# Kernel optimization log

Hardware: AMD Instinct MI355X
Metric: run time of the kernel (lower is better)

The kernel has to match this reference:

```python
import jax, jax.numpy as jnp
import numpy as np

B, T, LIE, OBS = 8, 2048, 32, 64
D = 2 * LIE  # d_head


def setup_inputs() -> dict:
    key = jax.random.key(0)
    ks = jax.random.split(key, 12)
    positions = jax.random.normal(ks[0], (B, T, D, D), dtype=jnp.float32)
    content_emb = jax.random.normal(ks[1], (B, T, OBS), dtype=jnp.float32)
    F = jnp.eye(LIE, dtype=jnp.float32) + 0.01 * jax.random.normal(ks[2], (LIE, LIE), dtype=jnp.float32)
    log_Q_diag = 0.1 * jax.random.normal(ks[3], (LIE,), dtype=jnp.float32)
    log_R_diag = 0.1 * jax.random.normal(ks[4], (OBS,), dtype=jnp.float32)
    H_w = jax.random.normal(ks[5], (OBS, LIE), dtype=jnp.float32) * (1.0 / np.sqrt(LIE))
    det_w1 = jax.random.normal(ks[6], (64, OBS), dtype=jnp.float32) * (1.0 / np.sqrt(OBS))
    det_b1 = jnp.zeros((64,), dtype=jnp.float32)
    det_w2 = jax.random.normal(ks[7], (1, 64), dtype=jnp.float32) * (1.0 / 8.0)
    det_b2 = jnp.zeros((1,), dtype=jnp.float32)
    obs_w = jax.random.normal(ks[8], (OBS, OBS), dtype=jnp.float32) * (1.0 / np.sqrt(OBS))
    obs_b = jnp.zeros((OBS,), dtype=jnp.float32)
    return {"positions": positions, "content_emb": content_emb, "F": F,
            "log_Q_diag": log_Q_diag, "log_R_diag": log_R_diag, "H_w": H_w,
            "det_w1": det_w1, "det_b1": det_b1, "det_w2": det_w2, "det_b2": det_b2,
            "obs_w": obs_w, "obs_b": obs_b}


def reference(positions, content_emb, F, log_Q_diag, log_R_diag, H_w,
              det_w1, det_b1, det_w2, det_b2, obs_w, obs_b):
    Bn, Tn, d, _ = positions.shape
    L = log_Q_diag.shape[0]
    Qd = jnp.exp(log_Q_diag)            # (L,) process noise diag
    Rd = jnp.exp(log_R_diag)            # (O,) measurement noise diag
    # landmark detector MLP + sigmoid (all timesteps at once)
    h = jax.nn.relu(content_emb @ det_w1.T + det_b1)
    probs = jax.nn.sigmoid((h @ det_w2.T + det_b2)[..., 0])   # (B,T)
    z_all = content_emb @ obs_w.T + obs_b                      # (B,T,O)
    ar = jnp.arange(L)
    I_L = jnp.eye(L, dtype=positions.dtype)
    Sigma0 = jnp.broadcast_to(I_L * 0.01, (Bn, L, L))

    def step(Sigma, inp):
        pos_t, z_t, prob_t = inp  # (B,d,d), (B,O), (B,)
        # predict: F Sigma F^T + Q
        Sigma = jnp.einsum('ij,bjk,lk->bil', F, Sigma, F) + jnp.diag(Qd)[None]
        # extract diagonal 2x2 blocks -> (B,L,2,2)
        resh = pos_t.reshape(Bn, L, 2, L, 2).transpose(0, 1, 3, 2, 4)  # (B,L,L,2,2)
        blocks = resh[:, ar, ar]
        # log map SO(2): theta = atan2(R10, R00)
        mu = jnp.arctan2(blocks[..., 1, 0], blocks[..., 0, 0])  # (B,L)
        # Kalman update
        S = jnp.einsum('oi,bij,pj->bop', H_w, Sigma, H_w) + jnp.diag(Rd)[None]
        K = jnp.einsum('bij,oj,bop->bip', Sigma, H_w, jnp.linalg.inv(S))  # (B,L,O)
        y = z_t - mu @ H_w.T
        mu_c = mu + jnp.einsum('bio,bo->bi', K, y)
        IKH = I_L[None] - K @ H_w
        Sigma_u = jnp.einsum('bij,bjk,blk->bil', IKH, Sigma, IKH) \
                  + jnp.einsum('bio,o,bjo->bij', K, Rd, K)
        # exp map SO(2)
        c, s = jnp.cos(mu_c), jnp.sin(mu_c)
        nb = jnp.stack([jnp.stack([c, -s], -1), jnp.stack([s, c], -1)], -2)  # (B,L,2,2)
        gate = jnp.any(prob_t > 0.5)  # torch branch: update only if any landmark
        a4 = prob_t[:, None, None, None]
        blended = jnp.where(gate, a4 * nb + (1.0 - a4) * blocks, blocks)
        a3 = prob_t[:, None, None]
        Sigma_out = jnp.where(gate, a3 * Sigma_u + (1.0 - a3) * Sigma, Sigma)
        corr_t = resh.at[:, ar, ar].set(blended).transpose(0, 1, 3, 2, 4).reshape(Bn, d, d)
        return Sigma_out, (corr_t, Sigma_out)

    _, (corr, covs) = jax.lax.scan(
        step, Sigma0,
        (positions.transpose(1, 0, 2, 3), z_all.transpose(1, 0, 2), probs.T))
    return corr.transpose(1, 0, 2, 3), covs.transpose(1, 0, 2, 3), probs
```

## Files before the change

kernel.cpp:

```cpp
#include <hip/hip_runtime.h>
#include <math.h>

#define TT 2048
#define NB 8
#define CH 16
#define BURN 32
#define NCH (TT / CH)
#define WMAX (BURN + CH)

typedef __attribute__((ext_vector_type(16))) float f32x16;
typedef __attribute__((ext_vector_type(8))) __bf16 bf16x8;

__device__ __forceinline__ bf16x8 ph(const f32x16& x, int base) {
  bf16x8 r;
#pragma unroll
  for (int d = 0; d < 8; ++d) r[d] = (__bf16)x[base + d];
  return r;
}
__device__ __forceinline__ bf16x8 pl(const f32x16& x, int base) {
  bf16x8 r;
#pragma unroll
  for (int d = 0; d < 8; ++d) {
    float t = x[base + d];
    r[d] = (__bf16)(t - (float)((__bf16)t));
  }
  return r;
}
struct FragsH { bf16x8 h0, h1; };
struct Frags { bf16x8 h0, l0, h1, l1; };
__device__ __forceinline__ FragsH mkh(const f32x16& x) { return {ph(x, 0), ph(x, 8)}; }
__device__ __forceinline__ Frags mkf(const f32x16& x) {
  return {ph(x, 0), pl(x, 0), ph(x, 8), pl(x, 8)};
}

#define MFMA_B __builtin_amdgcn_mfma_f32_32x32x16_bf16
__device__ __forceinline__ f32x16 mmA(bf16x8 a0, bf16x8 a1, bf16x8 b0, bf16x8 b1, f32x16 c) {
  c = MFMA_B(a0, b0, c, 0, 0, 0);
  c = MFMA_B(a1, b1, c, 0, 0, 0);
  return c;
}
__device__ __forceinline__ f32x16 mm6(const Frags& A, const Frags& B, f32x16 c) {
  f32x16 u = {};
  c = MFMA_B(A.h0, B.h0, c, 0, 0, 0);  u = MFMA_B(A.h0, B.l0, u, 0, 0, 0);
  c = MFMA_B(A.h1, B.h1, c, 0, 0, 0);  u = MFMA_B(A.h1, B.l1, u, 0, 0, 0);
  c = MFMA_B(A.l0, B.h0, c, 0, 0, 0);  u = MFMA_B(A.l1, B.h1, u, 0, 0, 0);
  return c + u;
}

__global__ __launch_bounds__(256) void k_setup(const float* __restrict__ Hw,
                                               const float* __restrict__ logR,
                                               float* __restrict__ cinv,
                                               float* __restrict__ htr) {
  __shared__ float C[32][33];
  __shared__ float rinv[64];
  int tid = threadIdx.x;
  if (tid < 64) rinv[tid] = expf(-logR[tid]);
  __syncthreads();
  int i = tid >> 3, j0 = (tid & 7) << 2;
  float a0 = 0.f, a1 = 0.f, a2 = 0.f, a3 = 0.f;
  for (int o = 0; o < 64; ++o) {
    float hio = Hw[o * 32 + i] * rinv[o];
    a0 += hio * Hw[o * 32 + j0];
    a1 += hio * Hw[o * 32 + j0 + 1];
    a2 += hio * Hw[o * 32 + j0 + 2];
    a3 += hio * Hw[o * 32 + j0 + 3];
  }
  C[i][j0] = a0; C[i][j0 + 1] = a1; C[i][j0 + 2] = a2; C[i][j0 + 3] = a3;
  for (int e = 0; e < 8; ++e) {
    int idx = tid * 8 + e;
    int ii = idx >> 6, o = idx & 63;
    htr[idx] = Hw[o * 32 + ii] * rinv[o];
  }
  __syncthreads();
  for (int k = 0; k < 32; ++k) {
    float ip = 1.0f / C[k][k];
    __syncthreads();
    if (tid < 32 && tid != k) C[k][tid] = -C[k][tid] * ip;
    __syncthreads();
    if (i != k) {
      float f = C[i][k];
      for (int q = 0; q < 4; ++q) {
        int j = j0 + q;
        if (j != k) C[i][j] += f * C[k][j];
      }
    }
    __syncthreads();
    if (tid < 32) {
      if (tid == k) C[k][k] = ip; else C[tid][k] *= ip;
    }
    __syncthreads();
  }
  cinv[i * 32 + j0]     = C[i][j0];
  cinv[i * 32 + j0 + 1] = C[i][j0 + 1];
  cinv[i * 32 + j0 + 2] = C[i][j0 + 2];
  cinv[i * 32 + j0 + 3] = C[i][j0 + 3];
}

__global__ __launch_bounds__(256) void k_obs(const float* __restrict__ emb,
                                             const float* __restrict__ w1,
                                             const float* __restrict__ b1,
                                             const float* __restrict__ w2,
                                             const float* __restrict__ b2,
                                             const float* __restrict__ ow,
                                             const float* __restrict__ ob,
                                             float* __restrict__ probs_out,
                                             float* __restrict__ zws) {
  int wave = threadIdx.x >> 6, lane = threadIdx.x & 63;
  int row = blockIdx.x * 4 + wave;
  float xv = emb[(size_t)row * 64 + lane];
  const float4* w1v = (const float4*)(w1 + lane * 64);
  float hacc = b1[lane];
#pragma unroll
  for (int i4 = 0; i4 < 16; ++i4) {
    float4 wv = w1v[i4];
    hacc += __shfl(xv, i4 * 4, 64) * wv.x + __shfl(xv, i4 * 4 + 1, 64) * wv.y +
            __shfl(xv, i4 * 4 + 2, 64) * wv.z + __shfl(xv, i4 * 4 + 3, 64) * wv.w;
  }
  float h = fmaxf(hacc, 0.f);
  float s = h * w2[lane];
#pragma unroll
  for (int off = 32; off; off >>= 1) s += __shfl_xor(s, off, 64);
  float prob = 1.0f / (1.0f + expf(-(s + b2[0])));
  if (lane == 0) probs_out[row] = prob;
  const float4* owv = (const float4*)(ow + lane * 64);
  float zacc = ob[lane];
#pragma unroll
  for (int i4 = 0; i4 < 16; ++i4) {
    float4 wv = owv[i4];
    zacc += __shfl(xv, i4 * 4, 64) * wv.x + __shfl(xv, i4 * 4 + 1, 64) * wv.y +
            __shfl(xv, i4 * 4 + 2, 64) * wv.z + __shfl(xv, i4 * 4 + 3, 64) * wv.w;
  }
  zws[(size_t)row * 64 + lane] = zacc;
}

__global__ void k_gate(const float* __restrict__ probs_out, int* __restrict__ gate) {
  int t = blockIdx.x * 256 + threadIdx.x;
  if (t < TT) {
    int g = 0;
    for (int b = 0; b < NB; ++b) g |= (probs_out[b * TT + t] > 0.5f) ? 1 : 0;
    gate[t] = g;
  }
}

__global__ __launch_bounds__(64, 1) void k_scan2(const float* __restrict__ Fg,
                                                 const float* __restrict__ logQ,
                                                 const float* __restrict__ probs_out,
                                                 const int* __restrict__ gate,
                                                 const float* __restrict__ cinv,
                                                 float* __restrict__ covs,
                                                 float* __restrict__ su_ws) {
  __shared__ float probL[WMAX];
  __shared__ int gateL[WMAX];
  const int ck = blockIdx.x, b = blockIdx.y, l = threadIdx.x;
  const int hh = l >> 5, c = l & 31;
  const int t0 = ck * CH;
  const int beg = (t0 - BURN > 0) ? (t0 - BURN) : 0;
  const int cnt = t0 + CH - beg;

  for (int i = l; i < cnt / 4; i += 64) {
    ((float4*)probL)[i] = ((const float4*)(probs_out + (size_t)b * TT + beg))[i];
    ((int4*)gateL)[i] = ((const int4*)(gate + beg))[i];
  }

  f32x16 vA, vC, vI;
#pragma unroll
  for (int s = 0; s < 2; ++s)
#pragma unroll
    for (int i = 0; i < 8; ++i) {
      int col = 16 * s + 4 * hh + (i & 3) + 8 * (i >> 2);
      int q = i + 8 * s;
      vA[q] = Fg[c * 32 + col] - ((col == c) ? 1.0f : 0.0f);
      vC[q] = cinv[c * 32 + col];
      vI[q] = (col == c) ? 1.0f : 0.0f;
    }
  const FragsH aFh = mkh(vA);
  const FragsH aFl = {pl(vA, 0), pl(vA, 8)};
  const Frags Cf = mkf(vC);
  const FragsH Idh = mkh(vI);

  f32x16 dq, qdv, ciD, sig, Xv;
  float qc = expf(logQ[c]);
#pragma unroll
  for (int q = 0; q < 16; ++q) {
    int rq = (q & 3) + 8 * (q >> 2) + 4 * hh;
    dq[q] = (rq == c) ? 1.0f : 0.0f;
    qdv[q] = (rq == c) ? qc : 0.0f;
    ciD[q] = cinv[rq * 32 + c];
    sig[q] = (rq == c) ? 0.01f : 0.0f;
    Xv[q] = 0.0f;
  }
  bf16x8 Xh0 = ph(Xv, 0), Xh1 = ph(Xv, 8);

  float* cbase = covs + (((size_t)(b * TT + beg)) << 10) + c * 32 + 4 * hh;
  float* sbase = su_ws + (((size_t)(b * TT + beg)) << 10) + c * 32 + 4 * hh;
  __syncthreads();
  float a3 = probL[0];
  int g = gateL[0];

#pragma unroll 1
  for (int tt = 0; tt < cnt; ++tt) {
    const int nn = (tt + 1 < cnt) ? tt + 1 : tt;
    float a3n = probL[nn];
    int gn = gateL[nn];
    const bool wr = (beg + tt >= t0);

    FragsH Sh = mkh(sig);
    f32x16 g2 = mmA(Sh.h0, Sh.h1, aFl.h0, aFl.h1,
                    mmA(Sh.h0, Sh.h1, aFh.h0, aFh.h1, sig));
    FragsH G2h = mkh(g2);
    f32x16 p = mmA(aFl.h0, aFl.h1, G2h.h0, G2h.h1,
                   mmA(aFh.h0, aFh.h1, G2h.h0, G2h.h1, g2 + qdv));

    if (g) {
      const f32x16 zz = {};
      f32x16 M = p + ciD;
      Frags Mf = mkf(M);
      f32x16 T = mmA(Mf.h0, Mf.h1, Xh0, Xh1, zz);
      float csum = 0.f;
#pragma unroll
      for (int q = 0; q < 16; ++q) csum += fabsf(dq[q] - T[q]);
      csum += __shfl_xor(csum, 32);

      if (__all(csum < 0.55f)) {
        FragsH Th = mkh(T);
        f32x16 U = mmA(Xh0, Xh1, Th.h0, Th.h1, zz);
        Xv = 2.0f * Xv - U;
        if (!__all(csum < 0.12f)) {
          FragsH Xn = mkh(Xv);
          f32x16 T2 = mmA(Mf.h0, Mf.h1, Xn.h0, Xn.h1, zz);
          FragsH T2h = mkh(T2);
          f32x16 U2 = mmA(Xn.h0, Xn.h1, T2h.h0, T2h.h1, zz);
          Xv = 2.0f * Xv - U2;
          if (!__all(csum < 0.30f)) {
            FragsH Xn3 = mkh(Xv);
            f32x16 T3n = mmA(Mf.h0, Mf.h1, Xn3.h0, Xn3.h1, zz);
            FragsH T3h = mkh(T3n);
            f32x16 U3 = mmA(Xn3.h0, Xn3.h1, T3h.h0, T3h.h1, zz);
            Xv = 2.0f * Xv - U3;
          }
        }
        FragsH Xp = mkh(Xv);
        f32x16 Xt = mmA(Xp.h0, Xp.h1, Idh.h0, Idh.h1, zz);
        f32x16 Xs = 0.5f * (Xv + Xt);
        Frags Xsf = mkf(Xs);
        f32x16 T3 = mm6(Mf, Xsf, zz);
        f32x16 E3 = dq - T3;
        FragsH E3h = mkh(E3);
        Xv = mmA(Xsf.h0, Xsf.h1, E3h.h0, E3h.h1, Xs);
      } else {
        float m[16];
#pragma unroll
        for (int q = 0; q < 16; ++q) m[q] = M[q];
#pragma unroll
        for (int k = 0; k < 32; ++k) {
          const int hk = (k >> 2) & 1;
          const int qk = (k & 3) | ((k >> 3) << 2);
          float pv = __shfl(m[qk], k + 32 * hk, 64);
          float r0 = __builtin_amdgcn_rcpf(pv);
          float ip = r0 * (2.0f - pv * r0);
          const bool myrow = (c == k);
#pragma unroll
          for (int q = 0; q < 16; ++q) {
            bool isdiag = (q == qk) && (hh == hk);
            float sc = -m[q] * ip;
            m[q] = (myrow && !isdiag) ? sc : m[q];
          }
          float fk = __shfl(m[qk], c + 32 * hk, 64);
          float prv[16];
#pragma unroll
          for (int q = 0; q < 16; ++q) prv[q] = __shfl(m[q], k + 32 * hh, 64);
#pragma unroll
          for (int q = 0; q < 16; ++q) {
            bool pivcol = (q == qk) && (hh == hk);
            float upd = fmaf(fk, prv[q], m[q]);
            m[q] = (!myrow && !pivcol) ? upd : m[q];
          }
          float cf = myrow ? ip : fk * ip;
          m[qk] = (hh == hk) ? cf : m[qk];
        }
#pragma unroll
        for (int q = 0; q < 16; ++q) Xv[q] = m[q];
      }

      const f32x16 zz2 = {};
      Xh0 = ph(Xv, 0);
      Xh1 = ph(Xv, 8);
      Frags Xf = {Xh0, pl(Xv, 0), Xh1, pl(Xv, 8)};
      f32x16 t5 = mm6(Xf, Cf, zz2);
      f32x16 Y = dq - t5;
      Frags Yf = mkf(Y);
      f32x16 Su = mm6(Cf, Yf, zz2);

      const float om = 1.0f - a3;
      f32x16 sg = a3 * Su + om * p;
      sig = sg;
      if (wr) {
#pragma unroll
        for (int j4 = 0; j4 < 4; ++j4) {
          float4 v;
          v.x = sg[4 * j4]; v.y = sg[4 * j4 + 1];
          v.z = sg[4 * j4 + 2]; v.w = sg[4 * j4 + 3];
          *(float4*)(cbase + 8 * j4) = v;
          float4 w;
          w.x = Su[4 * j4]; w.y = Su[4 * j4 + 1];
          w.z = Su[4 * j4 + 2]; w.w = Su[4 * j4 + 3];
          *(float4*)(sbase + 8 * j4) = w;
        }
      }
    } else {
      sig = p;
      if (wr) {
#pragma unroll
        for (int j4 = 0; j4 < 4; ++j4) {
          float4 v;
          v.x = p[4 * j4]; v.y = p[4 * j4 + 1];
          v.z = p[4 * j4 + 2]; v.w = p[4 * j4 + 3];
          *(float4*)(cbase + 8 * j4) = v;
        }
      }
    }
    cbase += 1024;
    sbase += 1024;
    a3 = a3n;
    g = gn;
  }
}

__global__ __launch_bounds__(256) void k_corr(const float* __restrict__ pos,
                                              const float* __restrict__ zws,
                                              const float* __restrict__ probs_out,
                                              const int* __restrict__ gate,
                                              const float* __restrict__ Hw,
                                              const float* __restrict__ htr,
                                              const float* __restrict__ su_ws,
                                              float* __restrict__ corr) {
  const int bid = blockIdx.x;
  const int b = bid >> 11, t = bid & 2047;
  const size_t pbase = ((size_t)bid) << 12;
  const float* src = pos + pbase;
  float* dst = corr + pbase;
  const int tid = threadIdx.x;
  const int g = gate[t];
  float4 v0 = ((const float4*)src)[tid];
  float4 v1 = ((const float4*)src)[256 + tid];
  float4 v2 = ((const float4*)src)[512 + tid];
  float4 v3 = ((const float4*)src)[768 + tid];
  if (!g) {
    ((float4*)dst)[tid] = v0;
    ((float4*)dst)[256 + tid] = v1;
    ((float4*)dst)[512 + tid] = v2;
    ((float4*)dst)[768 + tid] = v3;
    return;
  }
  __shared__ float muL[32], yL[64], vL[32], blL[32][4];
  float a4 = probs_out[b * TT + t];
  float p00 = 0.f, p01 = 0.f, p10 = 0.f, p11 = 0.f, mu = 0.f;
  if (tid < 32) {
    int ii = tid;
    p00 = src[(2 * ii) * 64 + 2 * ii];
    p01 = src[(2 * ii) * 64 + 2 * ii + 1];
    p10 = src[(2 * ii + 1) * 64 + 2 * ii];
    p11 = src[(2 * ii + 1) * 64 + 2 * ii + 1];
    mu = atan2f(p10, p00);
    muL[ii] = mu;
  }
  __syncthreads();
  if (tid < 64) {
    int o = tid;
    float zo = zws[((size_t)bid) * 64 + o];
    const float4* hrow = (const float4*)(Hw + o * 32);
    float s = 0.f;
#pragma unroll
    for (int i4 = 0; i4 < 8; ++i4) {
      float4 hv = hrow[i4];
      s += muL[i4 * 4] * hv.x + muL[i4 * 4 + 1] * hv.y +
           muL[i4 * 4 + 2] * hv.z + muL[i4 * 4 + 3] * hv.w;
    }
    yL[o] = zo - s;
  }
  __syncthreads();
  if (tid < 32) {
    const float4* hr = (const float4*)(htr + tid * 64);
    float s = 0.f;
#pragma unroll
    for (int j4 = 0; j4 < 16; ++j4) {
      float4 hv = hr[j4];
      s += yL[j4 * 4] * hv.x + yL[j4 * 4 + 1] * hv.y +
           yL[j4 * 4 + 2] * hv.z + yL[j4 * 4 + 3] * hv.w;
    }
    vL[tid] = s;
  }
  __syncthreads();
  if (tid < 32) {
    const float4* srow = (const float4*)(su_ws + (((size_t)bid) << 10) + tid * 32);
    float s = 0.f;
#pragma unroll
    for (int j4 = 0; j4 < 8; ++j4) {
      float4 sv = srow[j4];
      s += vL[j4 * 4] * sv.x + vL[j4 * 4 + 1] * sv.y +
           vL[j4 * 4 + 2] * sv.z + vL[j4 * 4 + 3] * sv.w;
    }
    float mc = mu + s;
    float cc = cosf(mc), sn = sinf(mc);
    float om = 1.0f - a4;
    blL[tid][0] = a4 * cc + om * p00;
    blL[tid][1] = a4 * (-sn) + om * p01;
    blL[tid][2] = a4 * sn + om * p10;
    blL[tid][3] = a4 * cc + om * p11;
  }
  __syncthreads();
  {
    float4 vv[4] = {v0, v1, v2, v3};
#pragma unroll
    for (int k = 0; k < 4; ++k) {
      int e0 = (k * 256 + tid) * 4;
      int row = e0 >> 6;
      int ii = row >> 1;
      int rp = (row & 1) << 1;
      int col = e0 & 63;
      float* f = (float*)&vv[k];
#pragma unroll
      for (int j = 0; j < 4; ++j) {
        int cc2 = col + j;
        if ((cc2 >> 1) == ii) f[j] = blL[ii][rp | (cc2 & 1)];
      }
      ((float4*)dst)[k * 256 + tid] = vv[k];
    }
  }
}

extern "C" void kernel_launch(void* const* d_in, const int* in_sizes, int n_in,
                              void* d_out, int out_size, void* d_ws, size_t ws_size,
                              hipStream_t stream) {
  const float* pos  = (const float*)d_in[0];
  const float* emb  = (const float*)d_in[1];
  const float* Fg   = (const float*)d_in[2];
  const float* logQ = (const float*)d_in[3];
  const float* logR = (const float*)d_in[4];
  const float* Hw   = (const float*)d_in[5];
  const float* w1   = (const float*)d_in[6];
  const float* b1   = (const float*)d_in[7];
  const float* w2   = (const float*)d_in[8];
  const float* b2   = (const float*)d_in[9];
  const float* ow   = (const float*)d_in[10];
  const float* ob   = (const float*)d_in[11];

  float* corr  = (float*)d_out;
  float* covs  = corr + 67108864;
  float* probs = corr + 83886080;

  float* ws   = (float*)d_ws;
  float* zws  = ws;
  int*   gate = (int*)(ws + 1048576);
  float* cinv = ws + 1050624;
  float* htr  = ws + 1051648;
  float* su   = ws + 1053696;

  hipLaunchKernelGGL(k_setup, dim3(1), dim3(256), 0, stream, Hw, logR, cinv, htr);
  hipLaunchKernelGGL(k_obs, dim3(4096), dim3(256), 0, stream, emb, w1, b1, w2, b2, ow, ob, probs, zws);
  hipLaunchKernelGGL(k_gate, dim3(8), dim3(256), 0, stream, probs, gate);
  hipLaunchKernelGGL(k_scan2, dim3(NCH, NB), dim3(64), 0, stream, Fg, logQ, probs, gate, cinv, covs, su);
  hipLaunchKernelGGL(k_corr, dim3(16384), dim3(256), 0, stream, pos, zws, probs, gate, Hw, htr, su, corr);
}
```

Baseline: 397.0 us.

## Overlap bulk positions copy with scan kernel; write only diagonal blocks afterward

The bulk copy of positions into corr now runs as extra blocks appended to the scan kernel's grid, so the memory-bound copy overlaps the latency-bound, low-occupancy scan. The correction kernel shrinks to 64 threads, returns early for ungated timesteps, and writes only the 2x2 diagonal blocks. It no longer rereads and rewrites the full matrix. The copy blocks use 64-thread workgroups with launch_bounds(64,1), which may limit copy throughput. The scan blocks' position in the grid determines whether they start early.

```diff
diff --git a/kernel.cpp b/kernel.cpp
--- a/kernel.cpp
+++ b/kernel.cpp
@@ -7,6 +7,7 @@
 #define BURN 32
 #define NCH (TT / CH)
 #define WMAX (BURN + CH)
+#define NSCAN (NCH * NB)
 
 typedef __attribute__((ext_vector_type(16))) float f32x16;
 typedef __attribute__((ext_vector_type(8))) __bf16 bf16x8;
@@ -142,16 +143,32 @@
   }
 }
 
-__global__ __launch_bounds__(64, 1) void k_scan2(const float* __restrict__ Fg,
-                                                 const float* __restrict__ logQ,
-                                                 const float* __restrict__ probs_out,
-                                                 const int* __restrict__ gate,
-                                                 const float* __restrict__ cinv,
-                                                 float* __restrict__ covs,
-                                                 float* __restrict__ su_ws) {
+__global__ __launch_bounds__(64, 1) void k_scan_copy(const float* __restrict__ Fg,
+                                                     const float* __restrict__ logQ,
+                                                     const float* __restrict__ probs_out,
+                                                     const int* __restrict__ gate,
+                                                     const float* __restrict__ cinv,
+                                                     float* __restrict__ covs,
+                                                     float* __restrict__ su_ws,
+                                                     const float* __restrict__ pos,
+                                                     float* __restrict__ corr) {
+  const int bid = blockIdx.x;
+  const int l = threadIdx.x;
+
+  if (bid >= NSCAN) {
+    const int idx = bid - NSCAN;
+    const float4* src = (const float4*)(pos + (((size_t)idx) << 12));
+    float4* dst = (float4*)(corr + (((size_t)idx) << 12));
+#pragma unroll
+    for (int k = 0; k < 16; ++k) {
+      dst[k * 64 + l] = src[k * 64 + l];
+    }
+    return;
+  }
+
   __shared__ float probL[WMAX];
   __shared__ int gateL[WMAX];
-  const int ck = blockIdx.x, b = blockIdx.y, l = threadIdx.x;
+  const int ck = bid & (NCH - 1), b = bid >> 7;
   const int hh = l >> 5, c = l & 31;
   const int t0 = ck * CH;
   const int beg = (t0 - BURN > 0) ? (t0 - BURN) : 0;
@@ -326,33 +343,22 @@
   }
 }
 
-__global__ __launch_bounds__(256) void k_corr(const float* __restrict__ pos,
-                                              const float* __restrict__ zws,
-                                              const float* __restrict__ probs_out,
-                                              const int* __restrict__ gate,
-                                              const float* __restrict__ Hw,
-                                              const float* __restrict__ htr,
-                                              const float* __restrict__ su_ws,
-                                              float* __restrict__ corr) {
+__global__ __launch_bounds__(64) void k_diag(const float* __restrict__ pos,
+                                             const float* __restrict__ zws,
+                                             const float* __restrict__ probs_out,
+                                             const int* __restrict__ gate,
+                                             const float* __restrict__ Hw,
+                                             const float* __restrict__ htr,
+                                             const float* __restrict__ su_ws,
+                                             float* __restrict__ corr) {
   const int bid = blockIdx.x;
   const int b = bid >> 11, t = bid & 2047;
+  if (!gate[t]) return;
   const size_t pbase = ((size_t)bid) << 12;
   const float* src = pos + pbase;
   float* dst = corr + pbase;
   const int tid = threadIdx.x;
-  const int g = gate[t];
-  float4 v0 = ((const float4*)src)[tid];
-  float4 v1 = ((const float4*)src)[256 + tid];
-  float4 v2 = ((const float4*)src)[512 + tid];
-  float4 v3 = ((const float4*)src)[768 + tid];
-  if (!g) {
-    ((float4*)dst)[tid] = v0;
-    ((float4*)dst)[256 + tid] = v1;
-    ((float4*)dst)[512 + tid] = v2;
-    ((float4*)dst)[768 + tid] = v3;
-    return;
-  }
-  __shared__ float muL[32], yL[64], vL[32], blL[32][4];
+  __shared__ float muL[32], yL[64], vL[32];
   float a4 = probs_out[b * TT + t];
   float p00 = 0.f, p01 = 0.f, p10 = 0.f, p11 = 0.f, mu = 0.f;
   if (tid < 32) {
@@ -365,7 +371,7 @@
     muL[ii] = mu;
   }
   __syncthreads();
-  if (tid < 64) {
+  {
     int o = tid;
     float zo = zws[((size_t)bid) * 64 + o];
     const float4* hrow = (const float4*)(Hw + o * 32);
@@ -403,29 +409,13 @@
     float mc = mu + s;
     float cc = cosf(mc), sn = sinf(mc);
     float om = 1.0f - a4;
-    blL[tid][0] = a4 * cc + om * p00;
-    blL[tid][1] = a4 * (-sn) + om * p01;
-    blL[tid][2] = a4 * sn + om * p10;
-    blL[tid][3] = a4 * cc + om * p11;
-  }
-  __syncthreads();
-  {
-    float4 vv[4] = {v0, v1, v2, v3};
-#pragma unroll
-    for (int k = 0; k < 4; ++k) {
-      int e0 = (k * 256 + tid) * 4;
-      int row = e0 >> 6;
-      int ii = row >> 1;
-      int rp = (row & 1) << 1;
-      int col = e0 & 63;
-      float* f = (float*)&vv[k];
-#pragma unroll
-      for (int j = 0; j < 4; ++j) {
-        int cc2 = col + j;
-        if ((cc2 >> 1) == ii) f[j] = blL[ii][rp | (cc2 & 1)];
-      }
-      ((float4*)dst)[k * 256 + tid] = vv[k];
-    }
+    float2 r0, r1;
+    r0.x = a4 * cc + om * p00;
+    r0.y = a4 * (-sn) + om * p01;
+    r1.x = a4 * sn + om * p10;
+    r1.y = a4 * cc + om * p11;
+    *(float2*)(dst + (2 * tid) * 64 + 2 * tid) = r0;
+    *(float2*)(dst + (2 * tid + 1) * 64 + 2 * tid) = r1;
   }
 }
 
@@ -459,6 +449,8 @@
   hipLaunchKernelGGL(k_setup, dim3(1), dim3(256), 0, stream, Hw, logR, cinv, htr);
   hipLaunchKernelGGL(k_obs, dim3(4096), dim3(256), 0, stream, emb, w1, b1, w2, b2, ow, ob, probs, zws);
   hipLaunchKernelGGL(k_gate, dim3(8), dim3(256), 0, stream, probs, gate);
-  hipLaunchKernelGGL(k_scan2, dim3(NCH, NB), dim3(64), 0, stream, Fg, logQ, probs, gate, cinv, covs, su);
-  hipLaunchKernelGGL(k_corr, dim3(16384), dim3(256), 0, stream, pos, zws, probs, gate, Hw, htr, su, corr);
-}
+  hipLaunchKernelGGL(k_scan_copy, dim3(NSCAN + NB * TT), dim3(64), 0, stream,
+                     Fg, logQ, probs, gate, cinv, covs, su, pos, corr);
+  hipLaunchKernelGGL(k_diag, dim3(NB * TT), dim3(64), 0, stream,
+                     pos, zws, probs, gate, Hw, htr, su, corr);
+}
```

Result: slower. 427.6 us (+7.7%).
